# Performance work log

Measured on AMD Instinct MI355X. Metric: run time of the kernel, lower is better.

Reference implementation:

```python
import jax, jax.numpy as jnp
import numpy as np

N_NODES = 50000
N_EDGES = 800000
IN_CH = 256
OUT_CH = 128
HID = 2 * OUT_CH  # 256
N_GRAPHS = 64


def setup_inputs() -> dict:
    key = jax.random.key(0)
    k = jax.random.split(key, 8)
    x = jax.random.normal(k[0], (N_NODES, IN_CH), dtype=jnp.float32)
    edge_index = jax.random.randint(k[1], (2, N_EDGES), 0, N_NODES, dtype=jnp.int64)
    batch = jnp.sort(jax.random.randint(k[2], (N_NODES,), 0, N_GRAPHS, dtype=jnp.int64))
    # GCNConv parameters (glorot-ish init)
    W1 = jax.random.normal(k[3], (IN_CH, HID), dtype=jnp.float32) / np.sqrt(IN_CH)
    b1 = jnp.zeros((HID,), dtype=jnp.float32)
    W2 = jax.random.normal(k[4], (HID, OUT_CH), dtype=jnp.float32) / np.sqrt(HID)
    b2 = jnp.zeros((OUT_CH,), dtype=jnp.float32)
    return {"x": x, "W1": W1, "b1": b1, "W2": W2, "b2": b2,
            "edge_index": edge_index, "batch": batch}


def _gcn_conv(x, W, b, src, dst, n):
    """PyG GCNConv: transform, then sym-normalized aggregation with self-loops."""
    h = x @ W  # [N, F_out]
    # degree over destination nodes, including the added self-loop
    deg = jnp.zeros((n,), dtype=h.dtype).at[dst].add(1.0) + 1.0
    dinv = jax.lax.rsqrt(deg)
    norm = dinv[src] * dinv[dst]            # [E]
    agg = jnp.zeros_like(h).at[dst].add(h[src] * norm[:, None])
    agg = agg + h * (1.0 / deg)[:, None]    # self-loop contribution: deg_i^{-1}
    return agg + b


def reference(x, W1, b1, W2, b2, edge_index, batch):
    src, dst = edge_index[0], edge_index[1]
    # dropout is identity in eval mode (training=False)
    h = jax.nn.elu(_gcn_conv(x, W1, b1, src, dst, N_NODES))
    h = _gcn_conv(h, W2, b2, src, dst, N_NODES)
    # global mean pool over graphs
    ones = jnp.ones((N_NODES,), dtype=h.dtype)
    counts = jax.ops.segment_sum(ones, batch, num_segments=N_GRAPHS)
    sums = jax.ops.segment_sum(h, batch, num_segments=N_GRAPHS)
    return sums / jnp.maximum(counts, 1.0)[:, None]
```

## Files before the change

### kernel.cpp

```cpp
#include <hip/hip_runtime.h>
#include <hip/hip_bf16.h>

#define N_NODES 50000
#define N_EDGES 800000
#define IN_CH 256
#define HID 256
#define OUT_CH 128
#define N_GRAPHS 64
#define SCAN_BLOCKS 196
#define M_PAD 50048
#define POOL_CHUNK 32
#define POOL_BLOCKS ((N_NODES + POOL_CHUNK - 1) / POOL_CHUNK)
#define AGG1_HALF 12500

typedef __bf16 bf16x8 __attribute__((ext_vector_type(8)));
typedef float f32x4 __attribute__((ext_vector_type(4)));
typedef unsigned short u16x8 __attribute__((ext_vector_type(8)));

__device__ __forceinline__ float bf2f(unsigned short u) {
    union { unsigned int i; float f; } x; x.i = ((unsigned int)u) << 16; return x.f;
}
__device__ __forceinline__ unsigned short f2bf(float f) {
    union { float f; unsigned int i; } x; x.f = f;
    unsigned int r = x.i + 0x7FFFu + ((x.i >> 16) & 1u);
    return (unsigned short)(r >> 16);
}

__device__ __forceinline__ void load16(const void* g, void* l) {
    __builtin_amdgcn_global_load_lds(
        (const __attribute__((address_space(1))) void*)g,
        (__attribute__((address_space(3))) void*)l, 16, 0, 0);
}

__device__ __forceinline__ int rp(const int* __restrict__ rl,
                                  const int* __restrict__ boff, int i) {
    return rl[i] + boff[i >> 8];
}

__global__ __launch_bounds__(256) void count_kernel(const int* __restrict__ ei,
                                                    int* __restrict__ cnt) {
    int e = blockIdx.x * 256 + threadIdx.x;
    if (e < N_EDGES) atomicAdd(&cnt[ei[N_EDGES + e]], 1);
}

__global__ __launch_bounds__(256) void scan_a_kernel(const int* __restrict__ cnt,
                                                     int* __restrict__ rl,
                                                     int* __restrict__ blocksum,
                                                     float* __restrict__ dinv,
                                                     float* __restrict__ invdeg) {
    __shared__ int tmp[256];
    int t = threadIdx.x;
    int i = blockIdx.x * 256 + t;
    int v = (i < N_NODES) ? cnt[i] : 0;
    int x = v;
    tmp[t] = x;
    __syncthreads();
#pragma unroll
    for (int off = 1; off < 256; off <<= 1) {
        int y = (t >= off) ? tmp[t - off] : 0;
        __syncthreads();
        x += y;
        tmp[t] = x;
        __syncthreads();
    }
    if (i <= N_NODES) rl[i] = x - v;
    if (i < N_NODES) {
        float d = (float)v + 1.0f;
        dinv[i] = rsqrtf(d);
        invdeg[i] = 1.0f / d;
    }
    if (t == 255) blocksum[blockIdx.x] = x;
}

__global__ __launch_bounds__(256) void scanb_cvtw_kernel(
        const int* __restrict__ blocksum, int* __restrict__ blockoff,
        const float* __restrict__ W1, const float* __restrict__ W2,
        unsigned short* __restrict__ w1t, unsigned short* __restrict__ w2t) {
    int t = threadIdx.x;
    if (blockIdx.x < 384) {
        int i = blockIdx.x * 256 + t;
        if (i < HID * IN_CH) {
            int n = i >> 8, k = i & 255;
            w1t[i] = f2bf(W1[k * HID + n]);
        } else {
            int j = i - HID * IN_CH;
            int n = j >> 8, k = j & 255;
            w2t[j] = f2bf(W2[k * OUT_CH + n]);
        }
        return;
    }
    __shared__ int tmp[256];
    int v = (t < SCAN_BLOCKS) ? blocksum[t] : 0;
    int x = v;
    tmp[t] = x;
    __syncthreads();
#pragma unroll
    for (int off = 1; off < 256; off <<= 1) {
        int y = (t >= off) ? tmp[t - off] : 0;
        __syncthreads();
        x += y;
        tmp[t] = x;
        __syncthreads();
    }
    if (t < SCAN_BLOCKS) blockoff[t] = x - v;
}

__global__ __launch_bounds__(256) void fill_kernel(const int* __restrict__ ei,
                                                   const int* __restrict__ rl,
                                                   const int* __restrict__ boff,
                                                   int* __restrict__ fillp,
                                                   int2* __restrict__ edge2,
                                                   const float* __restrict__ dinv) {
    int e = blockIdx.x * 256 + threadIdx.x;
    if (e >= N_EDGES) return;
    int s = ei[e];
    int d = ei[N_EDGES + e];
    int p = rp(rl, boff, d) + atomicAdd(&fillp[d], 1);
    float w = dinv[s] * dinv[d];
    edge2[p] = make_int2(s, __float_as_int(w));
}

__global__ __launch_bounds__(256) void gemm_mfma_kernel(
        const unsigned short* __restrict__ A,
        const unsigned short* __restrict__ Bt,
        unsigned short* __restrict__ C,
        int N) {
    const int K = 256;
    __shared__ char As[8192];
    __shared__ char Bs[8192];
    int tid = threadIdx.x;
    int bm = blockIdx.x * 128;
    int bn = blockIdx.y * 128;
    int lane = tid & 63, wave = tid >> 6;
    int lane15 = lane & 15, quad = lane >> 4;
    int wm0 = (wave >> 1) << 6;
    int wn0 = (wave & 1) << 6;

    int s1 = tid, s2 = tid + 256;
    int r1 = s1 >> 2, q1 = (s1 & 3) ^ ((r1 >> 1) & 3);
    int r2 = s2 >> 2, q2 = (s2 & 3) ^ ((r2 >> 1) & 3);
    const char* gA1 = (const char*)(A + (size_t)(bm + r1) * K) + (q1 << 4);
    const char* gA2 = (const char*)(A + (size_t)(bm + r2) * K) + (q2 << 4);
    const char* gB1 = (const char*)(Bt + (size_t)(bn + r1) * K) + (q1 << 4);
    const char* gB2 = (const char*)(Bt + (size_t)(bn + r2) * K) + (q2 << 4);
    char* lA1 = As + (wave << 10);
    char* lA2 = As + 4096 + (wave << 10);
    char* lB1 = Bs + (wave << 10);
    char* lB2 = Bs + 4096 + (wave << 10);

    int swm = (lane15 >> 1) & 3;
    f32x4 acc[4][4];
#pragma unroll
    for (int mt = 0; mt < 4; mt++)
#pragma unroll
        for (int nt = 0; nt < 4; nt++)
            acc[mt][nt] = (f32x4){0.f, 0.f, 0.f, 0.f};

    for (int k0 = 0; k0 < K; k0 += 32) {
        __syncthreads();
        load16(gA1 + (k0 << 1), lA1);
        load16(gA2 + (k0 << 1), lA2);
        load16(gB1 + (k0 << 1), lB1);
        load16(gB2 + (k0 << 1), lB2);
        __syncthreads();
        bf16x8 af[4], bfr[4];
#pragma unroll
        for (int t = 0; t < 4; t++) {
            int ra = wm0 + t * 16 + lane15;
            af[t] = *(const bf16x8*)(As + ra * 64 + ((quad ^ swm) << 4));
            int rb = wn0 + t * 16 + lane15;
            bfr[t] = *(const bf16x8*)(Bs + rb * 64 + ((quad ^ swm) << 4));
        }
#pragma unroll
        for (int mt = 0; mt < 4; mt++)
#pragma unroll
            for (int nt = 0; nt < 4; nt++)
                acc[mt][nt] = __builtin_amdgcn_mfma_f32_16x16x32_bf16(
                    af[mt], bfr[nt], acc[mt][nt], 0, 0, 0);
    }

#pragma unroll
    for (int mt = 0; mt < 4; mt++) {
        int rowb = bm + wm0 + mt * 16 + quad * 4;
#pragma unroll
        for (int nt = 0; nt < 4; nt++) {
            int col = bn + wn0 + nt * 16 + lane15;
            f32x4 a = acc[mt][nt];
            C[(size_t)(rowb + 0) * N + col] = f2bf(a[0]);
            C[(size_t)(rowb + 1) * N + col] = f2bf(a[1]);
            C[(size_t)(rowb + 2) * N + col] = f2bf(a[2]);
            C[(size_t)(rowb + 3) * N + col] = f2bf(a[3]);
        }
    }
}

__global__ __launch_bounds__(256) void gemm_mfma_x_kernel(
        const float* __restrict__ A,
        const unsigned short* __restrict__ Bt,
        unsigned short* __restrict__ Ca,
        unsigned short* __restrict__ Cb) {
    const int K = 256;
    __shared__ char As[8192];
    __shared__ char Bs[8192];
    int tid = threadIdx.x;
    int bm = blockIdx.x * 128;
    int bn = blockIdx.y * 128;
    int lane = tid & 63, wave = tid >> 6;
    int lane15 = lane & 15, quad = lane >> 4;
    int wm0 = (wave >> 1) << 6;
    int wn0 = (wave & 1) << 6;

    int s1 = tid, s2 = tid + 256;
    int r1 = s1 >> 2, q1 = (s1 & 3) ^ ((r1 >> 1) & 3);
    int r2 = s2 >> 2, q2 = (s2 & 3) ^ ((r2 >> 1) & 3);
    const bool in1 = (bm + r1) < N_NODES;
    const bool in2 = (bm + r2) < N_NODES;
    const float* gA1 = A + (size_t)(bm + r1) * K + (q1 << 3);
    const float* gA2 = A + (size_t)(bm + r2) * K + (q2 << 3);
    const char* gB1 = (const char*)(Bt + (size_t)(bn + r1) * K) + (q1 << 4);
    const char* gB2 = (const char*)(Bt + (size_t)(bn + r2) * K) + (q2 << 4);
    char* lB1 = Bs + (wave << 10);
    char* lB2 = Bs + 4096 + (wave << 10);

    int swm = (lane15 >> 1) & 3;
    f32x4 acc[4][4];
#pragma unroll
    for (int mt = 0; mt < 4; mt++)
#pragma unroll
        for (int nt = 0; nt < 4; nt++)
            acc[mt][nt] = (f32x4){0.f, 0.f, 0.f, 0.f};

    const float4 z4 = make_float4(0.f, 0.f, 0.f, 0.f);
    for (int k0 = 0; k0 < K; k0 += 32) {
        __syncthreads();
        load16(gB1 + (k0 << 1), lB1);
        load16(gB2 + (k0 << 1), lB2);
        float4 a0 = in1 ? *(const float4*)(gA1 + k0)     : z4;
        float4 a1 = in1 ? *(const float4*)(gA1 + k0 + 4) : z4;
        float4 a2 = in2 ? *(const float4*)(gA2 + k0)     : z4;
        float4 a3 = in2 ? *(const float4*)(gA2 + k0 + 4) : z4;
        u16x8 u1 = { f2bf(a0.x), f2bf(a0.y), f2bf(a0.z), f2bf(a0.w),
                     f2bf(a1.x), f2bf(a1.y), f2bf(a1.z), f2bf(a1.w) };
        u16x8 u2 = { f2bf(a2.x), f2bf(a2.y), f2bf(a2.z), f2bf(a2.w),
                     f2bf(a3.x), f2bf(a3.y), f2bf(a3.z), f2bf(a3.w) };
        *(u16x8*)(As + s1 * 16) = u1;
        *(u16x8*)(As + s2 * 16) = u2;
        __syncthreads();
        bf16x8 af[4], bfr[4];
#pragma unroll
        for (int t = 0; t < 4; t++) {
            int ra = wm0 + t * 16 + lane15;
            af[t] = *(const bf16x8*)(As + ra * 64 + ((quad ^ swm) << 4));
            int rb = wn0 + t * 16 + lane15;
            bfr[t] = *(const bf16x8*)(Bs + rb * 64 + ((quad ^ swm) << 4));
        }
#pragma unroll
        for (int mt = 0; mt < 4; mt++)
#pragma unroll
            for (int nt = 0; nt < 4; nt++)
                acc[mt][nt] = __builtin_amdgcn_mfma_f32_16x16x32_bf16(
                    af[mt], bfr[nt], acc[mt][nt], 0, 0, 0);
    }

#pragma unroll
    for (int mt = 0; mt < 4; mt++) {
        int rowb = bm + wm0 + mt * 16 + quad * 4;
#pragma unroll
        for (int nt = 0; nt < 4; nt++) {
            int gc = bn + wn0 + nt * 16 + lane15;
            unsigned short* Cp = (gc & 128) ? Cb : Ca;
            int pc = gc & 127;
            f32x4 a = acc[mt][nt];
            Cp[(size_t)(rowb + 0) * 128 + pc] = f2bf(a[0]);
            Cp[(size_t)(rowb + 1) * 128 + pc] = f2bf(a[1]);
            Cp[(size_t)(rowb + 2) * 128 + pc] = f2bf(a[2]);
            Cp[(size_t)(rowb + 3) * 128 + pc] = f2bf(a[3]);
        }
    }
}

#define ACC2(V, W) \
    acc.x += bf2f(V.x) * W; acc.y += bf2f(V.y) * W;

__global__ __launch_bounds__(256) void agg1_kernel(const unsigned short* __restrict__ h1a,
                                                   const unsigned short* __restrict__ h1b,
                                                   const float* __restrict__ bias,
                                                   const int* __restrict__ rl,
                                                   const int* __restrict__ boff,
                                                   const int2* __restrict__ edge2,
                                                   const float* __restrict__ invdeg,
                                                   unsigned short* __restrict__ out) {
    int bx = blockIdx.x;
    int plane = (bx >= AGG1_HALF) ? 1 : 0;
    int node = (plane ? bx - AGG1_HALF : bx) * 4 + (threadIdx.x >> 6);
    int lane = threadIdx.x & 63;
    const ushort2* hp = (const ushort2*)(plane ? h1b : h1a);
    int co = plane << 7;
    float id = invdeg[node];
    ushort2 sv = hp[(size_t)node * 64 + lane];
    float2 acc = make_float2(bf2f(sv.x) * id, bf2f(sv.y) * id);
    int e0 = rp(rl, boff, node);
    int e1 = rp(rl, boff, node + 1);
    int e = e0;
    for (; e + 7 < e1; e += 8) {
        int2 ed[8];
        ushort2 v[8];
#pragma unroll
        for (int j = 0; j < 8; j++) ed[j] = edge2[e + j];
#pragma unroll
        for (int j = 0; j < 8; j++) v[j] = hp[(size_t)ed[j].x * 64 + lane];
#pragma unroll
        for (int j = 0; j < 8; j++) {
            float w = __int_as_float(ed[j].y);
            ACC2(v[j], w);
        }
    }
    for (; e + 3 < e1; e += 4) {
        int2 ed[4];
        ushort2 v[4];
#pragma unroll
        for (int j = 0; j < 4; j++) ed[j] = edge2[e + j];
#pragma unroll
        for (int j = 0; j < 4; j++) v[j] = hp[(size_t)ed[j].x * 64 + lane];
#pragma unroll
        for (int j = 0; j < 4; j++) {
            float w = __int_as_float(ed[j].y);
            ACC2(v[j], w);
        }
    }
    for (; e < e1; e++) {
        int2 ed0 = edge2[e];
        float w0 = __int_as_float(ed0.y);
        ushort2 v0 = hp[(size_t)ed0.x * 64 + lane];
        ACC2(v0, w0);
    }
    float2 bb = ((const float2*)(bias + co))[lane];
    acc.x += bb.x; acc.y += bb.y;
    acc.x = acc.x > 0.f ? acc.x : expm1f(acc.x);
    acc.y = acc.y > 0.f ? acc.y : expm1f(acc.y);
    ushort2 o;
    o.x = f2bf(acc.x); o.y = f2bf(acc.y);
    ((ushort2*)(out + (size_t)node * 256 + co))[lane] = o;
}

__global__ __launch_bounds__(256) void agg2_kernel(const unsigned short* __restrict__ h,
                                                   const float* __restrict__ bias,
                                                   const int* __restrict__ rl,
                                                   const int* __restrict__ boff,
                                                   const int2* __restrict__ edge2,
                                                   const float* __restrict__ invdeg,
                                                   unsigned short* __restrict__ out) {
    int node = blockIdx.x * 4 + (threadIdx.x >> 6);
    if (node >= N_NODES) return;
    int lane = threadIdx.x & 63;
    const ushort2* h2 = (const ushort2*)h;
    float id = invdeg[node];
    ushort2 sv = h2[(size_t)node * 64 + lane];
    float2 acc = make_float2(bf2f(sv.x) * id, bf2f(sv.y) * id);
    int e0 = rp(rl, boff, node);
    int e1 = rp(rl, boff, node + 1);
    int e = e0;
    for (; e + 7 < e1; e += 8) {
        int2 ed[8];
        ushort2 v[8];
#pragma unroll
        for (int j = 0; j < 8; j++) ed[j] = edge2[e + j];
#pragma unroll
        for (int j = 0; j < 8; j++) v[j] = h2[(size_t)ed[j].x * 64 + lane];
#pragma unroll
        for (int j = 0; j < 8; j++) {
            float w = __int_as_float(ed[j].y);
            ACC2(v[j], w);
        }
    }
    for (; e + 3 < e1; e += 4) {
        int2 ed[4];
        ushort2 v[4];
#pragma unroll
        for (int j = 0; j < 4; j++) ed[j] = edge2[e + j];
#pragma unroll
        for (int j = 0; j < 4; j++) v[j] = h2[(size_t)ed[j].x * 64 + lane];
#pragma unroll
        for (int j = 0; j < 4; j++) {
            float w = __int_as_float(ed[j].y);
            ACC2(v[j], w);
        }
    }
    for (; e < e1; e++) {
        int2 ed0 = edge2[e];
        float w0 = __int_as_float(ed0.y);
        ushort2 v0 = h2[(size_t)ed0.x * 64 + lane];
        ACC2(v0, w0);
    }
    float2 bb = ((const float2*)bias)[lane];
    acc.x += bb.x; acc.y += bb.y;
    ushort2 o;
    o.x = f2bf(acc.x); o.y = f2bf(acc.y);
    ((ushort2*)out)[(size_t)node * 64 + lane] = o;
}

__global__ __launch_bounds__(128) void pool_kernel(const unsigned short* __restrict__ h,
                                                   const int* __restrict__ batch,
                                                   float* __restrict__ pool,
                                                   float* __restrict__ gcnt) {
    int c = threadIdx.x;
    int n0 = blockIdx.x * POOL_CHUNK;
    int n1 = n0 + POOL_CHUNK;
    if (n1 > N_NODES) n1 = N_NODES;
    if (n0 >= N_NODES) return;
    float run = 0.f, cnt = 0.f;
    int g = batch[n0];
    for (int n = n0; n < n1; n++) {
        int gn = batch[n];
        if (gn != g) {
            atomicAdd(&pool[g * OUT_CH + c], run);
            if (c == 0) atomicAdd(&gcnt[g], cnt);
            run = 0.f; cnt = 0.f; g = gn;
        }
        run += bf2f(h[(size_t)n * OUT_CH + c]);
        if (c == 0) cnt += 1.f;
    }
    atomicAdd(&pool[g * OUT_CH + c], run);
    if (c == 0) atomicAdd(&gcnt[g], cnt);
}

__global__ __launch_bounds__(256) void final_kernel(const float* __restrict__ pool,
                                                    const float* __restrict__ gcnt,
                                                    float* __restrict__ out) {
    int i = blockIdx.x * 256 + threadIdx.x;
    if (i < N_GRAPHS * OUT_CH)
        out[i] = pool[i] / fmaxf(gcnt[i >> 7], 1.0f);
}

extern "C" void kernel_launch(void* const* d_in, const int* in_sizes, int n_in,
                              void* d_out, int out_size, void* d_ws, size_t ws_size,
                              hipStream_t stream) {
    const float* x  = (const float*)d_in[0];
    const float* W1 = (const float*)d_in[1];
    const float* b1 = (const float*)d_in[2];
    const float* W2 = (const float*)d_in[3];
    const float* b2 = (const float*)d_in[4];
    const int*   ei = (const int*)d_in[5];
    const int*   batch = (const int*)d_in[6];
    float* out = (float*)d_out;

    unsigned short* h1a = (unsigned short*)d_ws;
    unsigned short* h1b = h1a + (size_t)M_PAD * 128;
    unsigned short* hBb = h1b + (size_t)M_PAD * 128;
    unsigned short* h2b = hBb + (size_t)M_PAD * HID;
    unsigned short* w1t = h2b + (size_t)M_PAD * OUT_CH;
    unsigned short* w2t = w1t + HID * IN_CH;
    unsigned short* hcb = h1a;
    float* dinv   = (float*)(w2t + OUT_CH * HID);
    float* invdeg = dinv + N_NODES;
    int*   rl     = (int*)(invdeg + N_NODES);
    int2*  edge2  = (int2*)(rl + 50016);
    int*   cnt    = (int*)(edge2 + N_EDGES);
    int*   fillp  = cnt + N_NODES;
    float* gcnt   = (float*)(fillp + N_NODES);
    float* pool   = gcnt + N_GRAPHS;
    int*   blocksum = (int*)(pool + N_GRAPHS * OUT_CH);
    int*   blockoff = blocksum + 256;

    size_t zbytes = ((size_t)N_NODES * 2 + N_GRAPHS + (size_t)N_GRAPHS * OUT_CH) * 4;
    hipMemsetAsync(cnt, 0, zbytes, stream);

    count_kernel<<<(N_EDGES + 255) / 256, 256, 0, stream>>>(ei, cnt);
    scan_a_kernel<<<SCAN_BLOCKS, 256, 0, stream>>>(cnt, rl, blocksum, dinv, invdeg);
    scanb_cvtw_kernel<<<385, 256, 0, stream>>>(blocksum, blockoff, W1, W2, w1t, w2t);
    fill_kernel<<<(N_EDGES + 255) / 256, 256, 0, stream>>>(ei, rl, blockoff, fillp, edge2, dinv);

    dim3 g1(M_PAD / 128, HID / 128);
    gemm_mfma_x_kernel<<<g1, 256, 0, stream>>>(x, w1t, h1a, h1b);
    agg1_kernel<<<2 * AGG1_HALF, 256, 0, stream>>>(h1a, h1b, b1, rl, blockoff,
                                                   edge2, invdeg, hBb);

    dim3 g2(M_PAD / 128, OUT_CH / 128);
    gemm_mfma_kernel<<<g2, 256, 0, stream>>>(hBb, w2t, h2b, OUT_CH);
    agg2_kernel<<<(N_NODES + 3) / 4, 256, 0, stream>>>(h2b, b2, rl, blockoff,
                                                       edge2, invdeg, hcb);

    pool_kernel<<<POOL_BLOCKS, 128, 0, stream>>>(hcb, batch, pool, gcnt);
    final_kernel<<<(N_GRAPHS * OUT_CH + 255) / 256, 256, 0, stream>>>(pool, gcnt, out);
}
```

Baseline: 339.0 us.

## Pre-convert x to bf16, use generic GEMM, and aggregate full 256-wide rows

Adds a separate kernel that converts x to bf16 up front. The first GEMM now reuses the generic bf16 kernel and writes a single interleaved 256-column h1 instead of two 128-column planes. agg1 now processes a whole node row per wavefront using ushort4 (8-byte) gathers, replacing the two-plane split with 4-byte gathers. The cost is an extra pass over x and a larger bf16 workspace, in exchange for wider, fewer gather transactions and reading each edge list once instead of twice.

```diff
diff --git a/kernel.cpp b/kernel.cpp
--- a/kernel.cpp
+++ b/kernel.cpp
@@ -11,11 +11,9 @@
 #define M_PAD 50048
 #define POOL_CHUNK 32
 #define POOL_BLOCKS ((N_NODES + POOL_CHUNK - 1) / POOL_CHUNK)
-#define AGG1_HALF 12500
 
 typedef __bf16 bf16x8 __attribute__((ext_vector_type(8)));
 typedef float f32x4 __attribute__((ext_vector_type(4)));
-typedef unsigned short u16x8 __attribute__((ext_vector_type(8)));
 
 __device__ __forceinline__ float bf2f(unsigned short u) {
     union { unsigned int i; float f; } x; x.i = ((unsigned int)u) << 16; return x.f;
@@ -118,6 +116,20 @@
     int p = rp(rl, boff, d) + atomicAdd(&fillp[d], 1);
     float w = dinv[s] * dinv[d];
     edge2[p] = make_int2(s, __float_as_int(w));
+}
+
+__global__ __launch_bounds__(256) void cvt_x_kernel(const float* __restrict__ x,
+                                                    unsigned short* __restrict__ xb) {
+    int i = blockIdx.x * 256 + threadIdx.x;
+    if (i >= M_PAD * (IN_CH / 4)) return;
+    ushort4 o;
+    if (i < N_NODES * (IN_CH / 4)) {
+        float4 v = ((const float4*)x)[i];
+        o.x = f2bf(v.x); o.y = f2bf(v.y); o.z = f2bf(v.z); o.w = f2bf(v.w);
+    } else {
+        o = make_ushort4(0, 0, 0, 0);
+    }
+    ((ushort4*)xb)[i] = o;
 }
 
 __global__ __launch_bounds__(256) void gemm_mfma_kernel(
@@ -194,154 +206,73 @@
     }
 }
 
-__global__ __launch_bounds__(256) void gemm_mfma_x_kernel(
-        const float* __restrict__ A,
-        const unsigned short* __restrict__ Bt,
-        unsigned short* __restrict__ Ca,
-        unsigned short* __restrict__ Cb) {
-    const int K = 256;
-    __shared__ char As[8192];
-    __shared__ char Bs[8192];
-    int tid = threadIdx.x;
-    int bm = blockIdx.x * 128;
-    int bn = blockIdx.y * 128;
-    int lane = tid & 63, wave = tid >> 6;
-    int lane15 = lane & 15, quad = lane >> 4;
-    int wm0 = (wave >> 1) << 6;
-    int wn0 = (wave & 1) << 6;
-
-    int s1 = tid, s2 = tid + 256;
-    int r1 = s1 >> 2, q1 = (s1 & 3) ^ ((r1 >> 1) & 3);
-    int r2 = s2 >> 2, q2 = (s2 & 3) ^ ((r2 >> 1) & 3);
-    const bool in1 = (bm + r1) < N_NODES;
-    const bool in2 = (bm + r2) < N_NODES;
-    const float* gA1 = A + (size_t)(bm + r1) * K + (q1 << 3);
-    const float* gA2 = A + (size_t)(bm + r2) * K + (q2 << 3);
-    const char* gB1 = (const char*)(Bt + (size_t)(bn + r1) * K) + (q1 << 4);
-    const char* gB2 = (const char*)(Bt + (size_t)(bn + r2) * K) + (q2 << 4);
-    char* lB1 = Bs + (wave << 10);
-    char* lB2 = Bs + 4096 + (wave << 10);
-
-    int swm = (lane15 >> 1) & 3;
-    f32x4 acc[4][4];
-#pragma unroll
-    for (int mt = 0; mt < 4; mt++)
-#pragma unroll
-        for (int nt = 0; nt < 4; nt++)
-            acc[mt][nt] = (f32x4){0.f, 0.f, 0.f, 0.f};
-
-    const float4 z4 = make_float4(0.f, 0.f, 0.f, 0.f);
-    for (int k0 = 0; k0 < K; k0 += 32) {
-        __syncthreads();
-        load16(gB1 + (k0 << 1), lB1);
-        load16(gB2 + (k0 << 1), lB2);
-        float4 a0 = in1 ? *(const float4*)(gA1 + k0)     : z4;
-        float4 a1 = in1 ? *(const float4*)(gA1 + k0 + 4) : z4;
-        float4 a2 = in2 ? *(const float4*)(gA2 + k0)     : z4;
-        float4 a3 = in2 ? *(const float4*)(gA2 + k0 + 4) : z4;
-        u16x8 u1 = { f2bf(a0.x), f2bf(a0.y), f2bf(a0.z), f2bf(a0.w),
-                     f2bf(a1.x), f2bf(a1.y), f2bf(a1.z), f2bf(a1.w) };
-        u16x8 u2 = { f2bf(a2.x), f2bf(a2.y), f2bf(a2.z), f2bf(a2.w),
-                     f2bf(a3.x), f2bf(a3.y), f2bf(a3.z), f2bf(a3.w) };
-        *(u16x8*)(As + s1 * 16) = u1;
-        *(u16x8*)(As + s2 * 16) = u2;
-        __syncthreads();
-        bf16x8 af[4], bfr[4];
-#pragma unroll
-        for (int t = 0; t < 4; t++) {
-            int ra = wm0 + t * 16 + lane15;
-            af[t] = *(const bf16x8*)(As + ra * 64 + ((quad ^ swm) << 4));
-            int rb = wn0 + t * 16 + lane15;
-            bfr[t] = *(const bf16x8*)(Bs + rb * 64 + ((quad ^ swm) << 4));
-        }
-#pragma unroll
-        for (int mt = 0; mt < 4; mt++)
-#pragma unroll
-            for (int nt = 0; nt < 4; nt++)
-                acc[mt][nt] = __builtin_amdgcn_mfma_f32_16x16x32_bf16(
-                    af[mt], bfr[nt], acc[mt][nt], 0, 0, 0);
-    }
-
-#pragma unroll
-    for (int mt = 0; mt < 4; mt++) {
-        int rowb = bm + wm0 + mt * 16 + quad * 4;
-#pragma unroll
-        for (int nt = 0; nt < 4; nt++) {
-            int gc = bn + wn0 + nt * 16 + lane15;
-            unsigned short* Cp = (gc & 128) ? Cb : Ca;
-            int pc = gc & 127;
-            f32x4 a = acc[mt][nt];
-            Cp[(size_t)(rowb + 0) * 128 + pc] = f2bf(a[0]);
-            Cp[(size_t)(rowb + 1) * 128 + pc] = f2bf(a[1]);
-            Cp[(size_t)(rowb + 2) * 128 + pc] = f2bf(a[2]);
-            Cp[(size_t)(rowb + 3) * 128 + pc] = f2bf(a[3]);
-        }
-    }
-}
-
-#define ACC2(V, W) \
-    acc.x += bf2f(V.x) * W; acc.y += bf2f(V.y) * W;
-
-__global__ __launch_bounds__(256) void agg1_kernel(const unsigned short* __restrict__ h1a,
-                                                   const unsigned short* __restrict__ h1b,
+#define ACC4(V, W) \
+    acc.x += bf2f(V.x) * W; acc.y += bf2f(V.y) * W; \
+    acc.z += bf2f(V.z) * W; acc.w += bf2f(V.w) * W;
+
+__global__ __launch_bounds__(256) void agg1_kernel(const unsigned short* __restrict__ h,
                                                    const float* __restrict__ bias,
                                                    const int* __restrict__ rl,
                                                    const int* __restrict__ boff,
                                                    const int2* __restrict__ edge2,
                                                    const float* __restrict__ invdeg,
                                                    unsigned short* __restrict__ out) {
-    int bx = blockIdx.x;
-    int plane = (bx >= AGG1_HALF) ? 1 : 0;
-    int node = (plane ? bx - AGG1_HALF : bx) * 4 + (threadIdx.x >> 6);
+    int node = blockIdx.x * 4 + (threadIdx.x >> 6);
+    if (node >= N_NODES) return;
     int lane = threadIdx.x & 63;
-    const ushort2* hp = (const ushort2*)(plane ? h1b : h1a);
-    int co = plane << 7;
+    const ushort4* h4 = (const ushort4*)h;
     float id = invdeg[node];
-    ushort2 sv = hp[(size_t)node * 64 + lane];
-    float2 acc = make_float2(bf2f(sv.x) * id, bf2f(sv.y) * id);
+    ushort4 sv = h4[(size_t)node * 64 + lane];
+    float4 acc = make_float4(bf2f(sv.x) * id, bf2f(sv.y) * id,
+                             bf2f(sv.z) * id, bf2f(sv.w) * id);
     int e0 = rp(rl, boff, node);
     int e1 = rp(rl, boff, node + 1);
     int e = e0;
     for (; e + 7 < e1; e += 8) {
         int2 ed[8];
-        ushort2 v[8];
+        ushort4 v[8];
 #pragma unroll
         for (int j = 0; j < 8; j++) ed[j] = edge2[e + j];
 #pragma unroll
-        for (int j = 0; j < 8; j++) v[j] = hp[(size_t)ed[j].x * 64 + lane];
+        for (int j = 0; j < 8; j++) v[j] = h4[(size_t)ed[j].x * 64 + lane];
 #pragma unroll
         for (int j = 0; j < 8; j++) {
             float w = __int_as_float(ed[j].y);
-            ACC2(v[j], w);
+            ACC4(v[j], w);
         }
     }
     for (; e + 3 < e1; e += 4) {
         int2 ed[4];
-        ushort2 v[4];
+        ushort4 v[4];
 #pragma unroll
         for (int j = 0; j < 4; j++) ed[j] = edge2[e + j];
 #pragma unroll
-        for (int j = 0; j < 4; j++) v[j] = hp[(size_t)ed[j].x * 64 + lane];
+        for (int j = 0; j < 4; j++) v[j] = h4[(size_t)ed[j].x * 64 + lane];
 #pragma unroll
         for (int j = 0; j < 4; j++) {
             float w = __int_as_float(ed[j].y);
-            ACC2(v[j], w);
+            ACC4(v[j], w);
         }
     }
     for (; e < e1; e++) {
         int2 ed0 = edge2[e];
         float w0 = __int_as_float(ed0.y);
-        ushort2 v0 = hp[(size_t)ed0.x * 64 + lane];
-        ACC2(v0, w0);
-    }
-    float2 bb = ((const float2*)(bias + co))[lane];
-    acc.x += bb.x; acc.y += bb.y;
+        ushort4 v0 = h4[(size_t)ed0.x * 64 + lane];
+        ACC4(v0, w0);
+    }
+    float4 bb = ((const float4*)bias)[lane];
+    acc.x += bb.x; acc.y += bb.y; acc.z += bb.z; acc.w += bb.w;
     acc.x = acc.x > 0.f ? acc.x : expm1f(acc.x);
     acc.y = acc.y > 0.f ? acc.y : expm1f(acc.y);
-    ushort2 o;
-    o.x = f2bf(acc.x); o.y = f2bf(acc.y);
-    ((ushort2*)(out + (size_t)node * 256 + co))[lane] = o;
-}
+    acc.z = acc.z > 0.f ? acc.z : expm1f(acc.z);
+    acc.w = acc.w > 0.f ? acc.w : expm1f(acc.w);
+    ushort4 o;
+    o.x = f2bf(acc.x); o.y = f2bf(acc.y); o.z = f2bf(acc.z); o.w = f2bf(acc.w);
+    ((ushort4*)out)[(size_t)node * 64 + lane] = o;
+}
+
+#define ACC2(V, W) \
+    acc.x += bf2f(V.x) * W; acc.y += bf2f(V.y) * W;
 
 __global__ __launch_bounds__(256) void agg2_kernel(const unsigned short* __restrict__ h,
                                                    const float* __restrict__ bias,
@@ -444,13 +375,13 @@
     const int*   batch = (const int*)d_in[6];
     float* out = (float*)d_out;
 
-    unsigned short* h1a = (unsigned short*)d_ws;
-    unsigned short* h1b = h1a + (size_t)M_PAD * 128;
-    unsigned short* hBb = h1b + (size_t)M_PAD * 128;
+    unsigned short* xb  = (unsigned short*)d_ws;
+    unsigned short* h1b = xb  + (size_t)M_PAD * IN_CH;
+    unsigned short* hBb = h1b + (size_t)M_PAD * HID;
     unsigned short* h2b = hBb + (size_t)M_PAD * HID;
     unsigned short* w1t = h2b + (size_t)M_PAD * OUT_CH;
     unsigned short* w2t = w1t + HID * IN_CH;
-    unsigned short* hcb = h1a;
+    unsigned short* hcb = xb;
     float* dinv   = (float*)(w2t + OUT_CH * HID);
     float* invdeg = dinv + N_NODES;
     int*   rl     = (int*)(invdeg + N_NODES);
@@ -470,10 +401,11 @@
     scanb_cvtw_kernel<<<385, 256, 0, stream>>>(blocksum, blockoff, W1, W2, w1t, w2t);
     fill_kernel<<<(N_EDGES + 255) / 256, 256, 0, stream>>>(ei, rl, blockoff, fillp, edge2, dinv);
 
+    cvt_x_kernel<<<(M_PAD * (IN_CH / 4) + 255) / 256, 256, 0, stream>>>(x, xb);
     dim3 g1(M_PAD / 128, HID / 128);
-    gemm_mfma_x_kernel<<<g1, 256, 0, stream>>>(x, w1t, h1a, h1b);
-    agg1_kernel<<<2 * AGG1_HALF, 256, 0, stream>>>(h1a, h1b, b1, rl, blockoff,
-                                                   edge2, invdeg, hBb);
+    gemm_mfma_kernel<<<g1, 256, 0, stream>>>(xb, w1t, h1b, HID);
+    agg1_kernel<<<(N_NODES + 3) / 4, 256, 0, stream>>>(h1b, b1, rl, blockoff,
+                                                       edge2, invdeg, hBb);
 
     dim3 g2(M_PAD / 128, OUT_CH / 128);
     gemm_mfma_kernel<<<g2, 256, 0, stream>>>(hBb, w2t, h2b, OUT_CH);
```

Measured after the change: 321.9 us. 1.05x faster.
